# Kernel optimization log

Hardware: AMD Instinct MI355X
Metric: run time of the kernel (lower is better)

Reference implementation:

```python
import jax, jax.numpy as jnp
import numpy as np

B, T, H, DK, DV = 4, 2048, 1024, 1024, 1024


def setup_inputs() -> dict:
    key = jax.random.key(0)
    ks = jax.random.split(key, 9)
    s = lambda fan_in: 1.0 / np.sqrt(fan_in)
    return {
        "y_all": jax.random.normal(ks[0], (B, T, H), dtype=jnp.float32),
        "Wq": jax.random.uniform(ks[1], (H, DK), jnp.float32, -s(H), s(H)),
        "bq": jax.random.uniform(ks[2], (DK,), jnp.float32, -s(H), s(H)),
        "Wk": jax.random.uniform(ks[3], (H, DK), jnp.float32, -s(H), s(H)),
        "bk": jax.random.uniform(ks[4], (DK,), jnp.float32, -s(H), s(H)),
        "Wv": jax.random.uniform(ks[5], (H, DV), jnp.float32, -s(H), s(H)),
        "bv": jax.random.uniform(ks[6], (DV,), jnp.float32, -s(H), s(H)),
        "Wo": jax.random.uniform(ks[7], (DV, H), jnp.float32, -s(DV), s(DV)),
        "bo": jax.random.uniform(ks[8], (H,), jnp.float32, -s(DV), s(DV)),
    }


def reference(y_all, Wq, bq, Wk, bk, Wv, bv, Wo, bo):
    # Fused causal attention equivalent to the per-timestep Python loop.
    dk = Wq.shape[1]
    q = (y_all @ Wq + bq) / jnp.sqrt(jnp.asarray(dk, y_all.dtype))  # [B,T,DK]
    k = y_all @ Wk + bk                                             # [B,T,DK]
    v = y_all @ Wv + bv                                             # [B,T,DV]
    scores = jnp.einsum("bqd,bkd->bqk", q, k)                       # [B,T,T]
    t = y_all.shape[1]
    causal = jnp.tril(jnp.ones((t, t), dtype=bool))                 # [T,T]
    scores = jnp.where(causal[None], scores, jnp.asarray(-jnp.inf, scores.dtype))
    w = jax.nn.softmax(scores, axis=-1)                             # [B,T,T]
    ctx = jnp.einsum("bqk,bkd->bqd", w, v)                          # [B,T,DV]
    return ctx @ Wo + bo                                            # [B,T,H]
```

## Files before the change

kernel.cpp:

```cpp
#include <hip/hip_runtime.h>
#include <hip/hip_bf16.h>
#include <cstdint>

#define DEVI __device__ __forceinline__

typedef __attribute__((ext_vector_type(8))) short bf16x8;
typedef __attribute__((ext_vector_type(4))) short bf16x4;
typedef __attribute__((ext_vector_type(4))) float f32x4;

DEVI short f2bf(float f) {
  unsigned u = __float_as_uint(f);
  u += 0x7fff + ((u >> 16) & 1);
  return (short)(u >> 16);
}
DEVI float bf2f(short s) { return __uint_as_float(((unsigned)(unsigned short)s) << 16); }

DEVI void gl_lds16(const short* g, short* l) {
  __builtin_amdgcn_global_load_lds((const __attribute__((address_space(1))) unsigned*)g,
                                   (__attribute__((address_space(3))) unsigned*)l, 16, 0, 0);
}

constexpr int BM = 128, BN = 128, BK = 64;

template<int MODE, int BIASMODE, bool OUTF32, int DECODE>
__global__ __launch_bounds__(256, 2)
void gemm_bt(const short* __restrict__ A, const short* __restrict__ B,
             void* __restrict__ Cv, const float* __restrict__ b0,
             const float* __restrict__ b1, float scale,
             int K, int lda, int ldb, int ldc,
             long long sA, long long sB, long long sC, int tdim)
{
  const int nwg = gridDim.x, orig = blockIdx.x;
  const int q8 = nwg >> 3, r8 = nwg & 7;
  const int xcd = orig & 7, idx8 = orig >> 3;
  const int wg = (xcd < r8 ? xcd * (q8 + 1) : r8 * (q8 + 1) + (xcd - r8) * q8) + idx8;
  const int bz = blockIdx.z;

  int bi, bj;
  if constexpr (MODE == 4) {
    int b = (int)((__fsqrt_rn(8.f * (float)wg + 1.f) - 1.f) * 0.5f);
    if ((b + 1) * (b + 2) / 2 <= wg) ++b;
    if (b * (b + 1) / 2 > wg) --b;
    bi = b; bj = wg - b * (b + 1) / 2;
  } else {
    bi = wg / tdim;
    bj = wg - bi * tdim;
    if constexpr (DECODE == 3) { if (bz & 2) bi = (nwg / tdim) - 1 - bi; }
  }

  A += (long long)bz * sA;
  B += (long long)bz * sB;

  __shared__ __align__(16) short lA[2][BM * BK];
  __shared__ __align__(16) short lB[2][BN * BK];

  const int tid = threadIdx.x, wave = tid >> 6, lane = tid & 63;
  const int wr = wave >> 1, wc = wave & 1;
  const int brow = bi * BM, bcol = bj * BN;
  const int fr = lane & 15, h = lane >> 4;

  const int ck0 = ((h ^ (fr & 7))) * 8;
  const int swc = ((tid & 7) ^ ((tid >> 3) & 7)) * 8;
  const short* pA = A + (long long)(brow + (tid >> 3)) * lda + swc;
  const short* pB = B + (long long)(bcol + (tid >> 3)) * ldb + swc;

  f32x4 acc[4][4] = {};
  const int kend = (MODE == 2) ? (bi + 1) * BM : K;
  const int nt = kend / BK;

  auto stage = [&](int buf, int t) {
    const long long ko = (long long)t * BK;
#pragma unroll
    for (int j = 0; j < 4; ++j)
      gl_lds16(pA + (long long)(j * 32) * lda + ko, &lA[buf][j * 2048 + tid * 8]);
#pragma unroll
    for (int j = 0; j < 4; ++j)
      gl_lds16(pB + (long long)(j * 32) * ldb + ko, &lB[buf][j * 2048 + tid * 8]);
  };

  stage(0, 0);
  __syncthreads();

  int cur = 0;
  for (int t = 0; t < nt; ++t) {
    if (t + 1 < nt) stage(cur ^ 1, t + 1);

    const short* bufA = lA[cur];
    const short* bufB = lB[cur];
    bf16x8 af[4], bg[4];
#pragma unroll
    for (int m = 0; m < 4; ++m)
      af[m] = *(const bf16x8*)&bufA[(wr * 64 + m * 16 + fr) * BK + ck0];
#pragma unroll
    for (int n = 0; n < 4; ++n)
      bg[n] = *(const bf16x8*)&bufB[(wc * 64 + n * 16 + fr) * BK + ck0];
#pragma unroll
    for (int m = 0; m < 4; ++m)
#pragma unroll
      for (int n = 0; n < 4; ++n)
        acc[m][n] = __builtin_amdgcn_mfma_f32_16x16x32_bf16(af[m], bg[n], acc[m][n], 0, 0, 0);
#pragma unroll
    for (int m = 0; m < 4; ++m)
      af[m] = *(const bf16x8*)&bufA[((wr * 64 + m * 16 + fr) * BK + ck0) ^ 32];
#pragma unroll
    for (int n = 0; n < 4; ++n)
      bg[n] = *(const bf16x8*)&bufB[((wc * 64 + n * 16 + fr) * BK + ck0) ^ 32];
#pragma unroll
    for (int m = 0; m < 4; ++m)
#pragma unroll
      for (int n = 0; n < 4; ++n)
        acc[m][n] = __builtin_amdgcn_mfma_f32_16x16x32_bf16(af[m], bg[n], acc[m][n], 0, 0, 0);

    __syncthreads();
    cur ^= 1;
  }

  const int lrow = h * 4;
  float* Cf = (float*)Cv + (long long)bz * sC;
  short* Cs = (short*)Cv + (long long)bz * sC;
  int colg[4]; float bvv[4], scl[4];
#pragma unroll
  for (int n = 0; n < 4; ++n) {
    colg[n] = bcol + wc * 64 + n * 16 + fr;
    if constexpr (BIASMODE == 1) { bvv[n] = b0[colg[n]]; scl[n] = scale; }
    else if constexpr (BIASMODE == 2) {
      const int seg = colg[n] >> 10;
      bvv[n] = seg ? b1[colg[n] & 1023] : b0[colg[n] & 1023];
      scl[n] = seg ? 1.f : scale;
    } else { bvv[n] = 0.f; scl[n] = scale; }
  }
#pragma unroll
  for (int m = 0; m < 4; ++m) {
    const int row = brow + wr * 64 + m * 16 + lrow;
#pragma unroll
    for (int j = 0; j < 4; ++j) {
#pragma unroll
      for (int n = 0; n < 4; ++n) {
        const float val = (acc[m][n][j] + bvv[n]) * scl[n];
        if constexpr (OUTF32) Cf[(long long)(row + j) * ldc + colg[n]] = val;
        else                  Cs[(long long)(row + j) * ldc + colg[n]] = f2bf(val);
      }
    }
  }
}

__global__ __launch_bounds__(256)
void softmax_causal_bf16_k(short* __restrict__ sc)
{
  const int T = 2048;
  const long long row = blockIdx.x;
  const int t = (int)(row & (T - 1));
  short* ps = sc + row * (long long)T;
  const int tid = threadIdx.x, wave = tid >> 6, lane = tid & 63;
  const int c0 = tid * 8;
  const int wlim = ((t >> 7) + 1) << 7;

  bf16x8 v = {};
  if (c0 <= t) v = *(const bf16x8*)&ps[c0];
  float x[8];
#pragma unroll
  for (int j = 0; j < 8; ++j) x[j] = bf2f(v[j]);

  float mx = -3.0e38f;
#pragma unroll
  for (int j = 0; j < 8; ++j) if (c0 + j <= t) mx = fmaxf(mx, x[j]);
#pragma unroll
  for (int o = 32; o; o >>= 1) mx = fmaxf(mx, __shfl_xor(mx, o, 64));
  __shared__ float red[8];
  if (lane == 0) red[wave] = mx;
  __syncthreads();
  const float M = fmaxf(fmaxf(red[0], red[1]), fmaxf(red[2], red[3]));

  float e[8], s = 0.f;
#pragma unroll
  for (int j = 0; j < 8; ++j) { e[j] = (c0 + j <= t) ? __expf(x[j] - M) : 0.f; s += e[j]; }
#pragma unroll
  for (int o = 32; o; o >>= 1) s += __shfl_xor(s, o, 64);
  if (lane == 0) red[4 + wave] = s;
  __syncthreads();
  const float inv = 1.f / (red[4] + red[5] + red[6] + red[7]);

  if (c0 < wlim) {
    bf16x8 ov;
#pragma unroll
    for (int j = 0; j < 8; ++j) ov[j] = f2bf(e[j] * inv);
    *(bf16x8*)&ps[c0] = ov;
  }
}

__global__ __launch_bounds__(256)
void cvt_y_k(const float* __restrict__ y, short* __restrict__ ybf)
{
  const long long i = (long long)blockIdx.x * 256 + threadIdx.x;
  const float4 v0 = ((const float4*)y)[i * 2];
  const float4 v1 = ((const float4*)y)[i * 2 + 1];
  bf16x8 o;
  o[0] = f2bf(v0.x); o[1] = f2bf(v0.y); o[2] = f2bf(v0.z); o[3] = f2bf(v0.w);
  o[4] = f2bf(v1.x); o[5] = f2bf(v1.y); o[6] = f2bf(v1.z); o[7] = f2bf(v1.w);
  ((bf16x8*)ybf)[i] = o;
}

__global__ __launch_bounds__(256)
void cvt_w_all_k(const float* __restrict__ w0, const float* __restrict__ w1,
                 const float* __restrict__ w2, const float* __restrict__ w3,
                 short* __restrict__ o0, short* __restrict__ o1,
                 short* __restrict__ o2, short* __restrict__ o3)
{
  const int tx = threadIdx.x & 31, ty = threadIdx.x >> 5;
  const int r0 = blockIdx.y * 32, c0 = blockIdx.x * 32;
  if (blockIdx.z == 3) {
#pragma unroll
    for (int i = 0; i < 4; ++i)
      o3[(long long)(r0 + ty + 8 * i) * 1024 + c0 + tx] =
          f2bf(w3[(long long)(r0 + ty + 8 * i) * 1024 + c0 + tx]);
    return;
  }
  const float* in = (blockIdx.z == 0) ? w0 : (blockIdx.z == 1 ? w1 : w2);
  short* out      = (blockIdx.z == 0) ? o0 : (blockIdx.z == 1 ? o1 : o2);
  __shared__ float tile[32][33];
#pragma unroll
  for (int i = 0; i < 4; ++i)
    tile[ty + 8 * i][tx] = in[(long long)(r0 + ty + 8 * i) * 1024 + c0 + tx];
  __syncthreads();
#pragma unroll
  for (int i = 0; i < 4; ++i)
    out[(long long)(c0 + ty + 8 * i) * 1024 + r0 + tx] = f2bf(tile[tx][ty + 8 * i]);
}

__global__ __launch_bounds__(256)
void bias_init_k(const float* __restrict__ bo, float* __restrict__ outb)
{
  const int j = blockIdx.x * 256 + threadIdx.x;
  outb[j] = bo[j];
}

__global__ __launch_bounds__(256)
void bias_fold_k(const float* __restrict__ bv, const float* __restrict__ Wo,
                 float* __restrict__ outb)
{
  const int r0 = blockIdx.x * 16;
  const int c4 = threadIdx.x;
  float4 acc = make_float4(0.f, 0.f, 0.f, 0.f);
  for (int r = 0; r < 16; ++r) {
    const float s = bv[r0 + r];
    const float4 w = ((const float4*)(Wo + (long long)(r0 + r) * 1024))[c4];
    acc.x += s * w.x; acc.y += s * w.y; acc.z += s * w.z; acc.w += s * w.w;
  }
  atomicAdd(&outb[c4 * 4 + 0], acc.x);
  atomicAdd(&outb[c4 * 4 + 1], acc.y);
  atomicAdd(&outb[c4 * 4 + 2], acc.z);
  atomicAdd(&outb[c4 * 4 + 3], acc.w);
}

__global__ __launch_bounds__(256)
void combine4_k(const float* __restrict__ p, short* __restrict__ out)
{
  const long long i = (long long)blockIdx.x * 256 + threadIdx.x;
  const float4 a = ((const float4*)p)[i];
  const float4 b = ((const float4*)(p + 1048576))[i];
  const float4 c = ((const float4*)(p + 2097152))[i];
  const float4 d = ((const float4*)(p + 3145728))[i];
  bf16x4 o;
  o[0] = f2bf(a.x + b.x + c.x + d.x);
  o[1] = f2bf(a.y + b.y + c.y + d.y);
  o[2] = f2bf(a.z + b.z + c.z + d.z);
  o[3] = f2bf(a.w + b.w + c.w + d.w);
  ((bf16x4*)out)[i] = o;
}

extern "C" void kernel_launch(void* const* d_in, const int* in_sizes, int n_in,
                              void* d_out, int out_size, void* d_ws, size_t ws_size,
                              hipStream_t stream)
{
  (void)in_sizes; (void)n_in; (void)out_size; (void)ws_size;
  const float* y  = (const float*)d_in[0];
  const float* Wq = (const float*)d_in[1];
  const float* bq = (const float*)d_in[2];
  const float* Wk = (const float*)d_in[3];
  const float* bk = (const float*)d_in[4];
  const float* Wv = (const float*)d_in[5];
  const float* bv = (const float*)d_in[6];
  const float* Wo = (const float*)d_in[7];
  const float* bo = (const float*)d_in[8];
  float* out = (float*)d_out;

  const int T = 2048, H = 1024, DK = 1024;
  const long long MT = 8192;

  short* ws    = (short*)d_ws;
  short* ybf   = ws;
  short* WqkT  = ybf + MT * H;
  short* WoT   = WqkT + 2ll * 1024 * 1024;
  short* WvBf  = WoT + 1024ll * 1024;
  short* WvoT  = WvBf + 1024ll * 1024;
  short* QKb   = WvoT + 1024ll * 1024;
  short* zT    = QKb + MT * 2048;
  short* scores = zT + MT * 1024;
  float* bvWoBo = (float*)(scores + 4ll * T * T);
  float* wvoPart = bvWoBo + 1024;

  cvt_y_k<<<4096, 256, 0, stream>>>(y, ybf);
  cvt_w_all_k<<<dim3(32, 32, 4), 256, 0, stream>>>(
      Wq, Wk, Wo, Wv, WqkT, WqkT + 1024ll * 1024, WoT, WvBf);
  bias_init_k<<<4, 256, 0, stream>>>(bo, bvWoBo);
  bias_fold_k<<<64, 256, 0, stream>>>(bv, Wo, bvWoBo);

  gemm_bt<0, 0, true, 0><<<dim3(64, 1, 4), 256, 0, stream>>>(
      WoT, WvBf, wvoPart, nullptr, nullptr, 1.f, 256, 1024, 1024, 1024,
      256, 256, 1048576, 8);
  combine4_k<<<1024, 256, 0, stream>>>(wvoPart, WvoT);

  gemm_bt<0, 2, false, 0><<<dim3(64 * 16, 1, 1), 256, 0, stream>>>(
      ybf, WqkT, QKb, bq, bk, 1.f / 32.f, H, H, H, 2048, 0, 0, 0, 16);

  gemm_bt<0, 0, false, 0><<<dim3(512, 1, 1), 256, 0, stream>>>(
      WvoT, ybf, zT, nullptr, nullptr, 1.f, 1024, 1024, 1024, 8192,
      0, 0, 0, 64);

  gemm_bt<4, 0, false, 0><<<dim3(136, 1, 4), 256, 0, stream>>>(
      QKb, QKb + 1024, scores, nullptr, nullptr, 1.f, DK, 2048, 2048, T,
      (long long)T * 2048, (long long)T * 2048, (long long)T * T, 16);

  softmax_causal_bf16_k<<<(int)MT, 256, 0, stream>>>(scores);

  gemm_bt<2, 1, true, 3><<<dim3(16 * 8, 1, 4), 256, 0, stream>>>(
      scores, zT, out, bvWoBo, nullptr, 1.f, T, T, 8192, 1024,
      (long long)T * T, 2048, 2048ll * 1024, 8);
}
```

Baseline: 193.0 us.

## Fold Wq·Wkᵀ into a single matrix and drop key-side bias terms

Reformulates the scores algebraically: instead of projecting both Q and K (a 2048-wide GEMM over all tokens), it precomputes M = Wk·Wqᵀ from the weights and G = (y·M + Wk·bq)/32, then computes scores as G·yᵀ. Key-bias and q·bk terms are constant per query row and cancel in the softmax, so bk is ignored. This replaces the 8192x2048x1024 QK projection with a small weight GEMM plus an 8192x1024x1024 GEMM. It adds a GEMV and an extra partial-sum reduction, and it changes where bf16 rounding happens, which may shift accuracy.

```diff
diff --git a/kernel.cpp b/kernel.cpp
--- a/kernel.cpp
+++ b/kernel.cpp
@@ -26,8 +26,7 @@
 __global__ __launch_bounds__(256, 2)
 void gemm_bt(const short* __restrict__ A, const short* __restrict__ B,
              void* __restrict__ Cv, const float* __restrict__ b0,
-             const float* __restrict__ b1, float scale,
-             int K, int lda, int ldb, int ldc,
+             float scale, int K, int lda, int ldb, int ldc,
              long long sA, long long sB, long long sC, int tdim)
 {
   const int nwg = gridDim.x, orig = blockIdx.x;
@@ -118,16 +117,11 @@
   const int lrow = h * 4;
   float* Cf = (float*)Cv + (long long)bz * sC;
   short* Cs = (short*)Cv + (long long)bz * sC;
-  int colg[4]; float bvv[4], scl[4];
+  int colg[4]; float bvv[4];
 #pragma unroll
   for (int n = 0; n < 4; ++n) {
     colg[n] = bcol + wc * 64 + n * 16 + fr;
-    if constexpr (BIASMODE == 1) { bvv[n] = b0[colg[n]]; scl[n] = scale; }
-    else if constexpr (BIASMODE == 2) {
-      const int seg = colg[n] >> 10;
-      bvv[n] = seg ? b1[colg[n] & 1023] : b0[colg[n] & 1023];
-      scl[n] = seg ? 1.f : scale;
-    } else { bvv[n] = 0.f; scl[n] = scale; }
+    bvv[n] = (BIASMODE == 1) ? b0[colg[n]] : 0.f;
   }
 #pragma unroll
   for (int m = 0; m < 4; ++m) {
@@ -136,7 +130,7 @@
     for (int j = 0; j < 4; ++j) {
 #pragma unroll
       for (int n = 0; n < 4; ++n) {
-        const float val = (acc[m][n][j] + bvv[n]) * scl[n];
+        const float val = (acc[m][n][j] + bvv[n]) * scale;
         if constexpr (OUTF32) Cf[(long long)(row + j) * ldc + colg[n]] = val;
         else                  Cs[(long long)(row + j) * ldc + colg[n]] = f2bf(val);
       }
@@ -208,23 +202,23 @@
 {
   const int tx = threadIdx.x & 31, ty = threadIdx.x >> 5;
   const int r0 = blockIdx.y * 32, c0 = blockIdx.x * 32;
-  if (blockIdx.z == 3) {
+  if (blockIdx.z != 2) {
+    const float* in = (blockIdx.z == 0) ? w0 : (blockIdx.z == 1 ? w1 : w3);
+    short* out      = (blockIdx.z == 0) ? o0 : (blockIdx.z == 1 ? o1 : o3);
 #pragma unroll
     for (int i = 0; i < 4; ++i)
-      o3[(long long)(r0 + ty + 8 * i) * 1024 + c0 + tx] =
-          f2bf(w3[(long long)(r0 + ty + 8 * i) * 1024 + c0 + tx]);
+      out[(long long)(r0 + ty + 8 * i) * 1024 + c0 + tx] =
+          f2bf(in[(long long)(r0 + ty + 8 * i) * 1024 + c0 + tx]);
     return;
   }
-  const float* in = (blockIdx.z == 0) ? w0 : (blockIdx.z == 1 ? w1 : w2);
-  short* out      = (blockIdx.z == 0) ? o0 : (blockIdx.z == 1 ? o1 : o2);
   __shared__ float tile[32][33];
 #pragma unroll
   for (int i = 0; i < 4; ++i)
-    tile[ty + 8 * i][tx] = in[(long long)(r0 + ty + 8 * i) * 1024 + c0 + tx];
+    tile[ty + 8 * i][tx] = w2[(long long)(r0 + ty + 8 * i) * 1024 + c0 + tx];
   __syncthreads();
 #pragma unroll
   for (int i = 0; i < 4; ++i)
-    out[(long long)(c0 + ty + 8 * i) * 1024 + r0 + tx] = f2bf(tile[tx][ty + 8 * i]);
+    o2[(long long)(c0 + ty + 8 * i) * 1024 + r0 + tx] = f2bf(tile[tx][ty + 8 * i]);
 }
 
 __global__ __launch_bounds__(256)
@@ -250,6 +244,22 @@
   atomicAdd(&outb[c4 * 4 + 1], acc.y);
   atomicAdd(&outb[c4 * 4 + 2], acc.z);
   atomicAdd(&outb[c4 * 4 + 3], acc.w);
+}
+
+__global__ __launch_bounds__(256)
+void wkbq_gemv_k(const float* __restrict__ Wk, const float* __restrict__ bq,
+                 float* __restrict__ w)
+{
+  const int row = blockIdx.x, tid = threadIdx.x;
+  const float4 a = ((const float4*)(Wk + (long long)row * 1024))[tid];
+  const float4 b = ((const float4*)bq)[tid];
+  float s = a.x * b.x + a.y * b.y + a.z * b.z + a.w * b.w;
+#pragma unroll
+  for (int o = 32; o; o >>= 1) s += __shfl_xor(s, o, 64);
+  __shared__ float red[4];
+  if ((tid & 63) == 0) red[tid >> 6] = s;
+  __syncthreads();
+  if (tid == 0) w[row] = red[0] + red[1] + red[2] + red[3];
 }
 
 __global__ __launch_bounds__(256)
@@ -283,47 +293,59 @@
   const float* Wo = (const float*)d_in[7];
   const float* bo = (const float*)d_in[8];
   float* out = (float*)d_out;
-
-  const int T = 2048, H = 1024, DK = 1024;
+  (void)bk;
+
+  const int T = 2048;
   const long long MT = 8192;
+  const long long MM = 1048576;
 
   short* ws    = (short*)d_ws;
   short* ybf   = ws;
-  short* WqkT  = ybf + MT * H;
-  short* WoT   = WqkT + 2ll * 1024 * 1024;
-  short* WvBf  = WoT + 1024ll * 1024;
-  short* WvoT  = WvBf + 1024ll * 1024;
-  short* QKb   = WvoT + 1024ll * 1024;
-  short* zT    = QKb + MT * 2048;
+  short* WqBf  = ybf + MT * 1024;
+  short* WkBf  = WqBf + MM;
+  short* WoT   = WkBf + MM;
+  short* WvBf  = WoT + MM;
+  short* MTb   = WvBf + MM;
+  short* WvoT  = MTb + MM;
+  short* G     = WvoT + MM;
+  short* zT    = G + MT * 1024;
   short* scores = zT + MT * 1024;
   float* bvWoBo = (float*)(scores + 4ll * T * T);
-  float* wvoPart = bvWoBo + 1024;
+  float* wvec   = bvWoBo + 1024;
+  float* part   = wvec + 1024;
 
   cvt_y_k<<<4096, 256, 0, stream>>>(y, ybf);
   cvt_w_all_k<<<dim3(32, 32, 4), 256, 0, stream>>>(
-      Wq, Wk, Wo, Wv, WqkT, WqkT + 1024ll * 1024, WoT, WvBf);
+      Wq, Wk, Wo, Wv, WqBf, WkBf, WoT, WvBf);
   bias_init_k<<<4, 256, 0, stream>>>(bo, bvWoBo);
   bias_fold_k<<<64, 256, 0, stream>>>(bv, Wo, bvWoBo);
+  wkbq_gemv_k<<<1024, 256, 0, stream>>>(Wk, bq, wvec);
 
   gemm_bt<0, 0, true, 0><<<dim3(64, 1, 4), 256, 0, stream>>>(
-      WoT, WvBf, wvoPart, nullptr, nullptr, 1.f, 256, 1024, 1024, 1024,
+      WoT, WvBf, part, nullptr, 1.f, 256, 1024, 1024, 1024,
       256, 256, 1048576, 8);
-  combine4_k<<<1024, 256, 0, stream>>>(wvoPart, WvoT);
-
-  gemm_bt<0, 2, false, 0><<<dim3(64 * 16, 1, 1), 256, 0, stream>>>(
-      ybf, WqkT, QKb, bq, bk, 1.f / 32.f, H, H, H, 2048, 0, 0, 0, 16);
+  combine4_k<<<1024, 256, 0, stream>>>(part, WvoT);
+
+  gemm_bt<0, 0, true, 0><<<dim3(64, 1, 4), 256, 0, stream>>>(
+      WkBf, WqBf, part, nullptr, 1.f, 256, 1024, 1024, 1024,
+      256, 256, 1048576, 8);
+  combine4_k<<<1024, 256, 0, stream>>>(part, MTb);
 
   gemm_bt<0, 0, false, 0><<<dim3(512, 1, 1), 256, 0, stream>>>(
-      WvoT, ybf, zT, nullptr, nullptr, 1.f, 1024, 1024, 1024, 8192,
+      WvoT, ybf, zT, nullptr, 1.f, 1024, 1024, 1024, 8192,
       0, 0, 0, 64);
 
+  gemm_bt<0, 1, false, 0><<<dim3(512, 1, 1), 256, 0, stream>>>(
+      ybf, MTb, G, wvec, 1.f / 32.f, 1024, 1024, 1024, 1024,
+      0, 0, 0, 8);
+
   gemm_bt<4, 0, false, 0><<<dim3(136, 1, 4), 256, 0, stream>>>(
-      QKb, QKb + 1024, scores, nullptr, nullptr, 1.f, DK, 2048, 2048, T,
-      (long long)T * 2048, (long long)T * 2048, (long long)T * T, 16);
+      G, ybf, scores, nullptr, 1.f, 1024, 1024, 1024, T,
+      (long long)T * 1024, (long long)T * 1024, (long long)T * T, 16);
 
   softmax_causal_bf16_k<<<(int)MT, 256, 0, stream>>>(scores);
 
   gemm_bt<2, 1, true, 3><<<dim3(16 * 8, 1, 4), 256, 0, stream>>>(
-      scores, zT, out, bvWoBo, nullptr, 1.f, T, T, 8192, 1024,
+      scores, zT, out, bvWoBo, 1.f, T, T, 8192, 1024,
       (long long)T * T, 2048, 2048ll * 1024, 8);
 }
```

New measurement: 192.5 us. No clear change (-0.2%).
